# Kernel tuning notes

Hardware: AMD Instinct MI355X
Metric: run time of the kernel (lower is better)

## Reference

```python
import jax, jax.numpy as jnp
import numpy as np

B, N, T, H = 16, 512, 100, 64

def setup_inputs() -> dict:
    key = jax.random.key(0)
    ks = jax.random.split(key, 9)
    s = 0.1
    return {
        "x": jax.random.normal(ks[0], (B, N, T), dtype=jnp.float32),
        "conv1_w": jax.random.normal(ks[1], (16, 1, 3), dtype=jnp.float32) * s,
        "conv1_b": jax.random.normal(ks[2], (16,), dtype=jnp.float32) * s,
        "conv2_w": jax.random.normal(ks[3], (32, 16, 3), dtype=jnp.float32) * s,
        "conv2_b": jax.random.normal(ks[4], (32,), dtype=jnp.float32) * s,
        "W_ih": jax.random.normal(ks[5], (3 * H, 32), dtype=jnp.float32) * s,
        "W_hh": jax.random.normal(ks[6], (3 * H, H), dtype=jnp.float32) * s,
        "b_ih": jax.random.normal(ks[7], (3 * H,), dtype=jnp.float32) * s,
        "b_hh": jax.random.normal(ks[8], (3 * H,), dtype=jnp.float32) * s,
    }

def _causal_conv_relu(h, w, b):
    # h: [BN, C_in, T]; left-pad (k-1)*dilation = 2 for causality
    y = jax.lax.conv_general_dilated(
        h, w, window_strides=(1,), padding=[(2, 0)],
        dimension_numbers=("NCH", "OIH", "NCH"))
    return jax.nn.relu(y + b[None, :, None])

def reference(x, conv1_w, conv1_b, conv2_w, conv2_b, W_ih, W_hh, b_ih, b_hh):
    b_, n_, t_ = x.shape
    h = x.reshape(b_ * n_, 1, t_)
    h = _causal_conv_relu(h, conv1_w, conv1_b)   # [BN, 16, T]
    h = _causal_conv_relu(h, conv2_w, conv2_b)   # [BN, 32, T]
    seq = h.transpose(0, 2, 1)                   # [BN, T, 32]
    # precompute input-to-gate projections for all timesteps: [BN, T, 3H]
    xp = jnp.einsum("btc,gc->btg", seq, W_ih) + b_ih
    hdim = W_hh.shape[1]

    def step(hprev, xt):
        gh = hprev @ W_hh.T + b_hh               # [BN, 3H]
        xr, xz, xn = jnp.split(xt, 3, axis=-1)
        hr, hz, hn = jnp.split(gh, 3, axis=-1)
        r = jax.nn.sigmoid(xr + hr)
        z = jax.nn.sigmoid(xz + hz)
        nn_ = jnp.tanh(xn + r * hn)
        hnew = (1.0 - z) * nn_ + z * hprev
        return hnew, None

    h0 = jnp.zeros((b_ * n_, hdim), dtype=x.dtype)
    hf, _ = jax.lax.scan(step, h0, xp.transpose(1, 0, 2))  # scan over T
    return hf.reshape(b_, n_, hdim)
```

## Files before the change

### kernel.cpp

```cpp
#include <hip/hip_runtime.h>
#include <stdint.h>

typedef __attribute__((ext_vector_type(8))) short s16x8;
typedef __attribute__((ext_vector_type(4))) float f32x4;

__device__ __forceinline__ short f2bf(float f){
  union { float f; uint32_t u; } v; v.f = f;
  uint32_t u = v.u;
  u += 0x7fffu + ((u >> 16) & 1u);
  return (short)(u >> 16);
}
__device__ __forceinline__ float sigm_fast(float x){
  float e = __builtin_amdgcn_exp2f(x * -1.44269504f);
  return __builtin_amdgcn_rcpf(1.f + e);
}
__device__ __forceinline__ float tanh_fast(float x){
  float e = __builtin_amdgcn_exp2f(x * 2.88539008f);
  return __builtin_fmaf(-2.f, __builtin_amdgcn_rcpf(e + 1.f), 1.f);
}

#define MFMA16(a, b, c) __builtin_amdgcn_mfma_f32_16x16x32_bf16((a), (b), (c), 0, 0, 0)

__global__ __launch_bounds__(256, 2) void te_fused(
    const float* __restrict__ x,
    const float* __restrict__ w1, const float* __restrict__ b1,
    const float* __restrict__ w2, const float* __restrict__ b2,
    const float* __restrict__ Wih, const float* __restrict__ Whh,
    const float* __restrict__ bih, const float* __restrict__ bhh,
    float* __restrict__ out)
{
  __shared__ float x_s[16 * 100];
  __shared__ short hA[2][16 * 72];
  __shared__ short c1b[16 * 328];
  __shared__ short s_b[16 * 640];

  const int tid  = threadIdx.x;
  const int lane = tid & 63;
  const int wv   = tid >> 6;
  const int l15  = lane & 15;
  const int lg   = lane >> 4;
  const int seq0 = blockIdx.x * 16;

  if ((blockIdx.x >> 8) & 1) __builtin_amdgcn_s_sleep(7);

  {
    const float4* gx = reinterpret_cast<const float4*>(x + (size_t)seq0 * 100);
    float4* sx = reinterpret_cast<float4*>(x_s);
    for (int i = tid; i < 400; i += 256) sx[i] = gx[i];
  }
  {
    int* p = reinterpret_cast<int*>(&hA[0][0]);
    for (int i = tid; i < 576; i += 256) p[i] = 0;
  }

  s16x8 WhhHi[3][2], WihHi[3];
  f32x4 bias_r, bias_z, bias_xn, bias_hn;
#pragma unroll
  for (int g = 0; g < 3; ++g) {
    const int n = 64 * g + 16 * wv + l15;
#pragma unroll
    for (int ks = 0; ks < 2; ++ks) {
      const float* p = Whh + n * 64 + ks * 32 + lg * 8;
#pragma unroll
      for (int j = 0; j < 8; ++j) WhhHi[g][ks][j] = f2bf(p[j]);
    }
    const float* q = Wih + n * 32 + lg * 8;
#pragma unroll
    for (int j = 0; j < 8; ++j) WihHi[g][j] = f2bf(q[j]);
    float bi = bih[n], bh = bhh[n];
    if (g == 0) { float v = bi + bh; bias_r  = (f32x4){v, v, v, v}; }
    if (g == 1) { float v = bi + bh; bias_z  = (f32x4){v, v, v, v}; }
    if (g == 2) { bias_xn = (f32x4){bi, bi, bi, bi};
                  bias_hn = (f32x4){bh, bh, bh, bh}; }
  }

  s16x8 cW2[2];
  f32x4 b2v4;
  {
    const int ch = 16 * (wv & 1) + l15;
    float bv = b2[ch];
    b2v4 = (f32x4){bv, bv, bv, bv};
#pragma unroll
    for (int ks = 0; ks < 2; ++ks) {
      s16x8 h8;
#pragma unroll
      for (int j = 0; j < 8; ++j) {
        const int k = ks * 32 + lg * 8 + j;
        const int g = k >> 4, ii = k & 15;
        h8[j] = (g < 3) ? f2bf(w2[ch * 48 + ii * 3 + g]) : (short)0;
      }
      cW2[ks] = h8;
    }
  }

  const int sl  = tid >> 4;
  const int chc = tid & 15;
  const float w1v0 = w1[chc * 3 + 0], w1v1 = w1[chc * 3 + 1], w1v2 = w1[chc * 3 + 2];
  const float b1v = b1[chc];

  const short* sRd  = &s_b[0]   + l15 * 40 + lg * 8;
  const short* hRd  = &hA[0][0] + l15 * 72 + lg * 8;
  short*       hWr  = &hA[0][0] + (lg * 4) * 72 + 16 * wv + l15;
  const short* c1Rd = &c1b[0]   + l15 * 328 + lg * 8;
  short*       sWr  = &s_b[0]   + (lg * 4) * 40 + (wv & 1) * 16 + l15;
  short*       c1Wr = &c1b[0]   + sl * 328 + chc;
  const float* xRd  = &x_s[sl * 100];
  const int    ub   = (wv >> 1) * 8;

  __syncthreads();

  float hreg[4] = {0.f, 0.f, 0.f, 0.f};

#define CONV1_PHASE(T0_, CLAMP_) do {                                         \
    float xa, xb;                                                             \
    if (CLAMP_) {                                                             \
      const int xi0 = (T0_) - 4, xi1 = (T0_) - 3;                             \
      xa = (xi0 < 0) ? 0.f : xRd[xi0 < 0 ? 0 : (xi0 > 99 ? 99 : xi0)];        \
      xb = (xi1 < 0) ? 0.f : xRd[xi1 < 0 ? 0 : (xi1 > 99 ? 99 : xi1)];        \
    } else {                                                                  \
      xa = xRd[(T0_) - 4]; xb = xRd[(T0_) - 3];                               \
    }                                                                         \
    _Pragma("unroll")                                                         \
    for (int i = 0; i < 19; ++i) {                                            \
      const int xi = (T0_) - 2 + i;                                           \
      float xc;                                                               \
      if (CLAMP_) {                                                           \
        const int idx = xi < 0 ? 0 : (xi > 99 ? 99 : xi);                     \
        xc = (xi < 0) ? 0.f : xRd[idx];                                       \
      } else {                                                                \
        xc = xRd[xi];                                                         \
      }                                                                       \
      float c = __builtin_fmaf(w1v0, xa,                                      \
                __builtin_fmaf(w1v1, xb,                                      \
                __builtin_fmaf(w1v2, xc, b1v)));                              \
      c = c > 0.f ? c : 0.f;                                                  \
      if (CLAMP_) c = (xi < 0) ? 0.f : c;                                     \
      uint32_t cu;                                                            \
      asm("v_cvt_pk_bf16_f32 %0, %1, %2" : "=v"(cu) : "v"(c), "v"(c));        \
      c1Wr[i * 16] = (short)(cu & 0xffff);                                    \
      xa = xb; xb = xc;                                                       \
    }                                                                         \
  } while (0)

#define CONV2_PHASE() do {                                                    \
    _Pragma("unroll")                                                         \
    for (int i = 0; i < 8; ++i) {                                             \
      const int u = ub + i;                                                   \
      s16x8 a0 = *reinterpret_cast<const s16x8*>(c1Rd + u * 16);              \
      s16x8 a1 = *reinterpret_cast<const s16x8*>(c1Rd + u * 16 + 32);         \
      f32x4 sa = MFMA16(a1, cW2[1], MFMA16(a0, cW2[0], b2v4));                \
      float m0 = sa[0] > 0.f ? sa[0] : 0.f;                                   \
      float m1 = sa[1] > 0.f ? sa[1] : 0.f;                                   \
      float m2 = sa[2] > 0.f ? sa[2] : 0.f;                                   \
      float m3 = sa[3] > 0.f ? sa[3] : 0.f;                                   \
      uint32_t u01, u23;                                                      \
      asm("v_cvt_pk_bf16_f32 %0, %1, %2" : "=v"(u01) : "v"(m0), "v"(m1));     \
      asm("v_cvt_pk_bf16_f32 %0, %1, %2" : "=v"(u23) : "v"(m2), "v"(m3));     \
      sWr[u * 640 +   0] = (short)(u01 & 0xffff);                             \
      sWr[u * 640 +  40] = (short)(u01 >> 16);                                \
      sWr[u * 640 +  80] = (short)(u23 & 0xffff);                             \
      sWr[u * 640 + 120] = (short)(u23 >> 16);                                \
    }                                                                         \
  } while (0)

#define GSTEP(TL) do {                                                        \
    const int rb_ = (TL) & 1, wb_ = rb_ ^ 1;                                  \
    s16x8 as_ = *reinterpret_cast<const s16x8*>(sRd + (TL) * 640);            \
    s16x8 ah0 = *reinterpret_cast<const s16x8*>(hRd + rb_ * 1152);            \
    s16x8 ah1 = *reinterpret_cast<const s16x8*>(hRd + rb_ * 1152 + 32);       \
    __builtin_amdgcn_s_setprio(1);                                            \
    f32x4 pr = MFMA16(as_, WihHi[0],                                          \
               MFMA16(ah1, WhhHi[0][1],                                       \
               MFMA16(ah0, WhhHi[0][0], bias_r)));                            \
    f32x4 pz = MFMA16(as_, WihHi[1],                                          \
               MFMA16(ah1, WhhHi[1][1],                                       \
               MFMA16(ah0, WhhHi[1][0], bias_z)));                            \
    f32x4 xn = MFMA16(as_, WihHi[2], bias_xn);                                \
    f32x4 hn = MFMA16(ah1, WhhHi[2][1],                                       \
               MFMA16(ah0, WhhHi[2][0], bias_hn));                            \
    __builtin_amdgcn_s_setprio(0);                                            \
    float hnew[4];                                                            \
    _Pragma("unroll")                                                         \
    for (int i2 = 0; i2 < 4; ++i2) {                                          \
      float r = sigm_fast(pr[i2]);                                            \
      float z = sigm_fast(pz[i2]);                                            \
      float tn = tanh_fast(__builtin_fmaf(r, hn[i2], xn[i2]));                \
      float h = __builtin_fmaf(z, hreg[i2] - tn, tn);                         \
      hreg[i2] = h; hnew[i2] = h;                                             \
    }                                                                         \
    uint32_t p01, p23;                                                        \
    asm("v_cvt_pk_bf16_f32 %0, %1, %2" : "=v"(p01) : "v"(hnew[0]), "v"(hnew[1])); \
    asm("v_cvt_pk_bf16_f32 %0, %1, %2" : "=v"(p23) : "v"(hnew[2]), "v"(hnew[3])); \
    hWr[wb_ * 1152 +   0] = (short)(p01 & 0xffff);                            \
    hWr[wb_ * 1152 +  72] = (short)(p01 >> 16);                               \
    hWr[wb_ * 1152 + 144] = (short)(p23 & 0xffff);                            \
    hWr[wb_ * 1152 + 216] = (short)(p23 >> 16);                               \
    __syncthreads();                                                          \
  } while (0)

#define G16 do { GSTEP(0);  GSTEP(1);  GSTEP(2);  GSTEP(3);                   \
                 GSTEP(4);  GSTEP(5);  GSTEP(6);  GSTEP(7);                   \
                 GSTEP(8);  GSTEP(9);  GSTEP(10); GSTEP(11);                  \
                 GSTEP(12); GSTEP(13); GSTEP(14); GSTEP(15); } while (0)

  CONV1_PHASE(0, true);
  __syncthreads();
  CONV2_PHASE();
  __syncthreads();
  G16;

#pragma unroll 1
  for (int k = 1; k < 6; ++k) {
    const int t0 = k * 16;
    CONV1_PHASE(t0, false);
    __syncthreads();
    CONV2_PHASE();
    __syncthreads();
    G16;
  }

  CONV1_PHASE(96, true);
  __syncthreads();
  CONV2_PHASE();
  __syncthreads();
  GSTEP(0); GSTEP(1); GSTEP(2); GSTEP(3);

#pragma unroll
  for (int i2 = 0; i2 < 4; ++i2) {
    out[(size_t)(seq0 + lg * 4 + i2) * 64 + 16 * wv + l15] = hreg[i2];
  }
}

extern "C" void kernel_launch(void* const* d_in, const int* in_sizes, int n_in,
                              void* d_out, int out_size, void* d_ws, size_t ws_size,
                              hipStream_t stream)
{
  (void)in_sizes; (void)n_in; (void)d_ws; (void)ws_size; (void)out_size;
  const float* x   = (const float*)d_in[0];
  const float* w1  = (const float*)d_in[1];
  const float* b1  = (const float*)d_in[2];
  const float* w2  = (const float*)d_in[3];
  const float* b2  = (const float*)d_in[4];
  const float* Wih = (const float*)d_in[5];
  const float* Whh = (const float*)d_in[6];
  const float* bih = (const float*)d_in[7];
  const float* bhh = (const float*)d_in[8];
  float* out = (float*)d_out;
  te_fused<<<512, 256, 0, stream>>>(x, w1, b1, w2, b2, Wih, Whh, bih, bhh, out);
}
```

Baseline: 73.55 us.

## Give each wave its own 4 sequences to drop per-step block barriers in GRU

The recurrent GRU loop is reorganised so that each wave owns 4 of the block's 16 sequences and computes all 192 gate outputs for them, instead of every wave computing a 16-column slice for all 16 sequences. The hidden state is exchanged only through a per-wave scratch buffer, so the __syncthreads after each timestep goes away. Wih fragments move to shared memory and Whh for all 12 tiles is held in registers, and the log2e scaling is folded into the weights and biases ahead of time. In exchange, three quarters of the MFMA output rows are wasted, each step issues four times as many MFMAs, and register pressure rises sharply.

```diff
diff --git a/kernel.cpp b/kernel.cpp
--- a/kernel.cpp
+++ b/kernel.cpp
@@ -9,14 +9,6 @@
   uint32_t u = v.u;
   u += 0x7fffu + ((u >> 16) & 1u);
   return (short)(u >> 16);
-}
-__device__ __forceinline__ float sigm_fast(float x){
-  float e = __builtin_amdgcn_exp2f(x * -1.44269504f);
-  return __builtin_amdgcn_rcpf(1.f + e);
-}
-__device__ __forceinline__ float tanh_fast(float x){
-  float e = __builtin_amdgcn_exp2f(x * 2.88539008f);
-  return __builtin_fmaf(-2.f, __builtin_amdgcn_rcpf(e + 1.f), 1.f);
 }
 
 #define MFMA16(a, b, c) __builtin_amdgcn_mfma_f32_16x16x32_bf16((a), (b), (c), 0, 0, 0)
@@ -30,9 +22,10 @@
     float* __restrict__ out)
 {
   __shared__ float x_s[16 * 100];
-  __shared__ short hA[2][16 * 72];
   __shared__ short c1b[16 * 328];
   __shared__ short s_b[16 * 640];
+  __shared__ short wihL[12 * 64 * 8];
+  __shared__ float hscr[4][4 * 68];
 
   const int tid  = threadIdx.x;
   const int lane = tid & 63;
@@ -41,37 +34,42 @@
   const int lg   = lane >> 4;
   const int seq0 = blockIdx.x * 16;
 
-  if ((blockIdx.x >> 8) & 1) __builtin_amdgcn_s_sleep(7);
-
   {
     const float4* gx = reinterpret_cast<const float4*>(x + (size_t)seq0 * 100);
     float4* sx = reinterpret_cast<float4*>(x_s);
     for (int i = tid; i < 400; i += 256) sx[i] = gx[i];
   }
-  {
-    int* p = reinterpret_cast<int*>(&hA[0][0]);
-    for (int i = tid; i < 576; i += 256) p[i] = 0;
-  }
-
-  s16x8 WhhHi[3][2], WihHi[3];
-  f32x4 bias_r, bias_z, bias_xn, bias_hn;
-#pragma unroll
-  for (int g = 0; g < 3; ++g) {
-    const int n = 64 * g + 16 * wv + l15;
+  for (int i = tid; i < 12 * 64; i += 256) {
+    const int tile = i >> 6, ln = i & 63;
+    const int n  = tile * 16 + (ln & 15);
+    const int k0 = (ln >> 4) * 8;
+    const float gs = (tile < 8) ? -1.44269504f : 2.88539008f;
+    short* dst = &wihL[i * 8];
+#pragma unroll
+    for (int j = 0; j < 8; ++j) dst[j] = f2bf(gs * Wih[n * 32 + k0 + j]);
+  }
+
+  s16x8 WhhB[12][2];
+#pragma unroll
+  for (int g = 0; g < 12; ++g) {
+    const float gs = (g < 8) ? -1.44269504f : 2.88539008f;
+    const int n = 16 * g + l15;
 #pragma unroll
     for (int ks = 0; ks < 2; ++ks) {
       const float* p = Whh + n * 64 + ks * 32 + lg * 8;
 #pragma unroll
-      for (int j = 0; j < 8; ++j) WhhHi[g][ks][j] = f2bf(p[j]);
+      for (int j = 0; j < 8; ++j) WhhB[g][ks][j] = f2bf(gs * p[j]);
     }
-    const float* q = Wih + n * 32 + lg * 8;
-#pragma unroll
-    for (int j = 0; j < 8; ++j) WihHi[g][j] = f2bf(q[j]);
-    float bi = bih[n], bh = bhh[n];
-    if (g == 0) { float v = bi + bh; bias_r  = (f32x4){v, v, v, v}; }
-    if (g == 1) { float v = bi + bh; bias_z  = (f32x4){v, v, v, v}; }
-    if (g == 2) { bias_xn = (f32x4){bi, bi, bi, bi};
-                  bias_hn = (f32x4){bh, bh, bh, bh}; }
+  }
+
+  float brL[4], bzL[4], bxnL[4], bhnL[4];
+#pragma unroll
+  for (int G = 0; G < 4; ++G) {
+    const int d = 16 * G + l15;
+    brL[G]  = -1.44269504f * (bih[d] + bhh[d]);
+    bzL[G]  = -1.44269504f * (bih[64 + d] + bhh[64 + d]);
+    bxnL[G] =  2.88539008f * bih[128 + d];
+    bhnL[G] =  2.88539008f * bhh[128 + d];
   }
 
   s16x8 cW2[2];
@@ -98,18 +96,21 @@
   const float w1v0 = w1[chc * 3 + 0], w1v1 = w1[chc * 3 + 1], w1v2 = w1[chc * 3 + 2];
   const float b1v = b1[chc];
 
-  const short* sRd  = &s_b[0]   + l15 * 40 + lg * 8;
-  const short* hRd  = &hA[0][0] + l15 * 72 + lg * 8;
-  short*       hWr  = &hA[0][0] + (lg * 4) * 72 + 16 * wv + l15;
-  const short* c1Rd = &c1b[0]   + l15 * 328 + lg * 8;
-  short*       sWr  = &s_b[0]   + (lg * 4) * 40 + (wv & 1) * 16 + l15;
-  short*       c1Wr = &c1b[0]   + sl * 328 + chc;
+  const short* c1Rd = &c1b[0] + l15 * 328 + lg * 8;
+  short*       sWr  = &s_b[0] + (lg * 4) * 40 + (wv & 1) * 16 + l15;
+  short*       c1Wr = &c1b[0] + sl * 328 + chc;
   const float* xRd  = &x_s[sl * 100];
   const int    ub   = (wv >> 1) * 8;
+  const short* sRdW = &s_b[0] + (wv * 4 + (l15 & 3)) * 40 + lg * 8;
+  float*       hscrW = &hscr[wv][0];
+  const bool lb0 = (lg & 1) != 0;
+  const bool lb1 = (lg & 2) != 0;
 
   __syncthreads();
 
-  float hreg[4] = {0.f, 0.f, 0.f, 0.f};
+  float hG[4] = {0.f, 0.f, 0.f, 0.f};
+  s16x8 ah0 = (s16x8){0, 0, 0, 0, 0, 0, 0, 0};
+  s16x8 ah1 = (s16x8){0, 0, 0, 0, 0, 0, 0, 0};
 
 #define CONV1_PHASE(T0_, CLAMP_) do {                                         \
     float xa, xb;                                                             \
@@ -163,71 +164,74 @@
     }                                                                         \
   } while (0)
 
-#define GSTEP(TL) do {                                                        \
-    const int rb_ = (TL) & 1, wb_ = rb_ ^ 1;                                  \
-    s16x8 as_ = *reinterpret_cast<const s16x8*>(sRd + (TL) * 640);            \
-    s16x8 ah0 = *reinterpret_cast<const s16x8*>(hRd + rb_ * 1152);            \
-    s16x8 ah1 = *reinterpret_cast<const s16x8*>(hRd + rb_ * 1152 + 32);       \
-    __builtin_amdgcn_s_setprio(1);                                            \
-    f32x4 pr = MFMA16(as_, WihHi[0],                                          \
-               MFMA16(ah1, WhhHi[0][1],                                       \
-               MFMA16(ah0, WhhHi[0][0], bias_r)));                            \
-    f32x4 pz = MFMA16(as_, WihHi[1],                                          \
-               MFMA16(ah1, WhhHi[1][1],                                       \
-               MFMA16(ah0, WhhHi[1][0], bias_z)));                            \
-    f32x4 xn = MFMA16(as_, WihHi[2], bias_xn);                                \
-    f32x4 hn = MFMA16(ah1, WhhHi[2][1],                                       \
-               MFMA16(ah0, WhhHi[2][0], bias_hn));                            \
-    __builtin_amdgcn_s_setprio(0);                                            \
-    float hnew[4];                                                            \
-    _Pragma("unroll")                                                         \
-    for (int i2 = 0; i2 < 4; ++i2) {                                          \
-      float r = sigm_fast(pr[i2]);                                            \
-      float z = sigm_fast(pz[i2]);                                            \
-      float tn = tanh_fast(__builtin_fmaf(r, hn[i2], xn[i2]));                \
-      float h = __builtin_fmaf(z, hreg[i2] - tn, tn);                         \
-      hreg[i2] = h; hnew[i2] = h;                                             \
-    }                                                                         \
-    uint32_t p01, p23;                                                        \
-    asm("v_cvt_pk_bf16_f32 %0, %1, %2" : "=v"(p01) : "v"(hnew[0]), "v"(hnew[1])); \
-    asm("v_cvt_pk_bf16_f32 %0, %1, %2" : "=v"(p23) : "v"(hnew[2]), "v"(hnew[3])); \
-    hWr[wb_ * 1152 +   0] = (short)(p01 & 0xffff);                            \
-    hWr[wb_ * 1152 +  72] = (short)(p01 >> 16);                               \
-    hWr[wb_ * 1152 + 144] = (short)(p23 & 0xffff);                            \
-    hWr[wb_ * 1152 + 216] = (short)(p23 >> 16);                               \
-    __syncthreads();                                                          \
-  } while (0)
-
-#define G16 do { GSTEP(0);  GSTEP(1);  GSTEP(2);  GSTEP(3);                   \
-                 GSTEP(4);  GSTEP(5);  GSTEP(6);  GSTEP(7);                   \
-                 GSTEP(8);  GSTEP(9);  GSTEP(10); GSTEP(11);                  \
-                 GSTEP(12); GSTEP(13); GSTEP(14); GSTEP(15); } while (0)
-
-  CONV1_PHASE(0, true);
-  __syncthreads();
-  CONV2_PHASE();
-  __syncthreads();
-  G16;
+#define SEL4(Q_) (lb1 ? (lb0 ? (Q_)[3] : (Q_)[2]) : (lb0 ? (Q_)[1] : (Q_)[0]))
 
 #pragma unroll 1
-  for (int k = 1; k < 6; ++k) {
+  for (int k = 0; k < 7; ++k) {
     const int t0 = k * 16;
-    CONV1_PHASE(t0, false);
+    const int NS = (k < 6) ? 16 : 4;
+
+    if (k == 0 || k == 6) CONV1_PHASE(t0, true);
+    else                  CONV1_PHASE(t0, false);
     __syncthreads();
     CONV2_PHASE();
     __syncthreads();
-    G16;
-  }
-
-  CONV1_PHASE(96, true);
-  __syncthreads();
-  CONV2_PHASE();
-  __syncthreads();
-  GSTEP(0); GSTEP(1); GSTEP(2); GSTEP(3);
-
-#pragma unroll
-  for (int i2 = 0; i2 < 4; ++i2) {
-    out[(size_t)(seq0 + lg * 4 + i2) * 64 + 16 * wv + l15] = hreg[i2];
+
+#pragma unroll 1
+    for (int tl = 0; tl < NS; ++tl) {
+      s16x8 sfrag = *reinterpret_cast<const s16x8*>(sRdW + tl * 640);
+      const f32x4 z4 = {0.f, 0.f, 0.f, 0.f};
+#pragma unroll
+      for (int G = 0; G < 4; ++G) {
+        s16x8 wr = *reinterpret_cast<const s16x8*>(&wihL[((G    ) * 64 + lane) * 8]);
+        s16x8 wz = *reinterpret_cast<const s16x8*>(&wihL[((G + 4) * 64 + lane) * 8]);
+        s16x8 wn = *reinterpret_cast<const s16x8*>(&wihL[((G + 8) * 64 + lane) * 8]);
+        __builtin_amdgcn_s_setprio(1);
+        f32x4 Qr = MFMA16(ah1, WhhB[G][1],
+                   MFMA16(ah0, WhhB[G][0],
+                   MFMA16(sfrag, wr, z4)));
+        f32x4 Qz = MFMA16(ah1, WhhB[G + 4][1],
+                   MFMA16(ah0, WhhB[G + 4][0],
+                   MFMA16(sfrag, wz, z4)));
+        f32x4 Qxn = MFMA16(sfrag, wn, z4);
+        f32x4 Qhn = MFMA16(ah1, WhhB[G + 8][1],
+                    MFMA16(ah0, WhhB[G + 8][0], z4));
+        __builtin_amdgcn_s_setprio(0);
+        float pr = SEL4(Qr)  + brL[G];
+        float pz = SEL4(Qz)  + bzL[G];
+        float xn = SEL4(Qxn) + bxnL[G];
+        float hn = SEL4(Qhn) + bhnL[G];
+        float r = __builtin_amdgcn_rcpf(1.f + __builtin_amdgcn_exp2f(pr));
+        float z = __builtin_amdgcn_rcpf(1.f + __builtin_amdgcn_exp2f(pz));
+        float arg = __builtin_fmaf(r, hn, xn);
+        float tn = __builtin_fmaf(-2.f,
+                   __builtin_amdgcn_rcpf(__builtin_amdgcn_exp2f(arg) + 1.f), 1.f);
+        float h = __builtin_fmaf(z, hG[G] - tn, tn);
+        hG[G] = h;
+        hscrW[lg * 68 + 16 * G + l15] = h;
+      }
+      const float* hrow = hscrW + (l15 & 3) * 68 + lg * 8;
+      f32x4 ha = *reinterpret_cast<const f32x4*>(hrow);
+      f32x4 hb = *reinterpret_cast<const f32x4*>(hrow + 4);
+      f32x4 hc = *reinterpret_cast<const f32x4*>(hrow + 32);
+      f32x4 hd = *reinterpret_cast<const f32x4*>(hrow + 36);
+      union { s16x8 v; uint32_t u[4]; } fa, fb;
+      asm("v_cvt_pk_bf16_f32 %0, %1, %2" : "=v"(fa.u[0]) : "v"(ha[0]), "v"(ha[1]));
+      asm("v_cvt_pk_bf16_f32 %0, %1, %2" : "=v"(fa.u[1]) : "v"(ha[2]), "v"(ha[3]));
+      asm("v_cvt_pk_bf16_f32 %0, %1, %2" : "=v"(fa.u[2]) : "v"(hb[0]), "v"(hb[1]));
+      asm("v_cvt_pk_bf16_f32 %0, %1, %2" : "=v"(fa.u[3]) : "v"(hb[2]), "v"(hb[3]));
+      asm("v_cvt_pk_bf16_f32 %0, %1, %2" : "=v"(fb.u[0]) : "v"(hc[0]), "v"(hc[1]));
+      asm("v_cvt_pk_bf16_f32 %0, %1, %2" : "=v"(fb.u[1]) : "v"(hc[2]), "v"(hc[3]));
+      asm("v_cvt_pk_bf16_f32 %0, %1, %2" : "=v"(fb.u[2]) : "v"(hd[0]), "v"(hd[1]));
+      asm("v_cvt_pk_bf16_f32 %0, %1, %2" : "=v"(fb.u[3]) : "v"(hd[2]), "v"(hd[3]));
+      ah0 = fa.v; ah1 = fb.v;
+    }
+  }
+
+  {
+    float* op = out + (size_t)(seq0 + wv * 4 + lg) * 64 + l15;
+#pragma unroll
+    for (int G = 0; G < 4; ++G) op[16 * G] = hG[G];
   }
 }
 
```

After: 142.8 us. +94.2%, slower.
